# Kernel optimization log

Measured on AMD Instinct MI355X. Metric: run time of the kernel, lower is better.

## Reference

```python
import jax, jax.numpy as jnp
import numpy as np

N_NODES = 100000
N_EDGES = 3200000
N_GRAPHS = 1000
HID = 64
L = 4  # num_unit


def setup_inputs() -> dict:
    key = jax.random.key(0)
    ks = jax.random.split(key, 16)
    x = jax.random.normal(ks[0], (N_NODES, 4), dtype=jnp.float32)
    edge_index = jax.random.randint(ks[1], (2, N_EDGES), 0, N_NODES, dtype=jnp.int64)
    edge_attr = jax.random.uniform(ks[2], (N_EDGES,), dtype=jnp.float32)
    batch = jnp.sort(jax.random.randint(ks[3], (N_NODES,), 0, N_GRAPHS, dtype=jnp.int64))
    s = 1.0 / np.sqrt(HID)
    inp = {
        'x': x, 'edge_index': edge_index, 'edge_attr': edge_attr, 'batch': batch,
        'emb_w': jax.random.normal(ks[4], (4, HID), jnp.float32) * 0.5,
        'emb_b': jnp.zeros((HID,), jnp.float32),
        'conv_w1': jax.random.normal(ks[5], (L, HID, HID), jnp.float32) * s,
        'conv_b1': jnp.zeros((L, HID), jnp.float32),
        'conv_w2': jax.random.normal(ks[6], (L, HID, HID), jnp.float32) * s,
        'conv_w3': jax.random.normal(ks[7], (L, HID, HID), jnp.float32) * s,
        'conv_b3': jnp.zeros((L, HID), jnp.float32),
        'lin1_w': jax.random.normal(ks[8], (HID, HID), jnp.float32) * s,
        'lin1_b': jnp.zeros((HID,), jnp.float32),
        'lin2_w': jax.random.normal(ks[9], (HID, 3), jnp.float32) * s,
        'lin2_b': jnp.zeros((3,), jnp.float32),
    }
    return inp


def _forward(x, edge_index, edge_attr, batch,
             emb_w, emb_b, conv_w1, conv_b1, conv_w2, conv_w3, conv_b3,
             lin1_w, lin1_b, lin2_w, lin2_b):
    src, dst = edge_index[0], edge_index[1]
    ew = edge_attr[:, None]  # [E,1]
    h = x @ emb_w + emb_b  # node_emb; dropout omitted (eval mode)
    for l in range(conv_w1.shape[0]):
        # LEConv: out_i = sum_{j->i} w_ji * (lin1(x_j) - lin2(x_i)) + lin3(x_i)
        a = h @ conv_w1[l] + conv_b1[l]
        b = h @ conv_w2[l]  # no bias
        msg = (a[src] - b[dst]) * ew  # [E, HID]
        agg = jax.ops.segment_sum(msg, dst, num_segments=h.shape[0])
        h = jax.nn.relu(agg + h @ conv_w3[l] + conv_b3[l])
    # global mean pool over graphs
    sums = jax.ops.segment_sum(h, batch, num_segments=N_GRAPHS)
    cnt = jax.ops.segment_sum(jnp.ones((h.shape[0],), h.dtype), batch, num_segments=N_GRAPHS)
    graph_x = sums / jnp.maximum(cnt, 1.0)[:, None]
    pred = jax.nn.relu(graph_x @ lin1_w + lin1_b) @ lin2_w + lin2_b
    return pred


def reference(x, edge_index, edge_attr, batch, emb_w, emb_b,
              conv_w1, conv_b1, conv_w2, conv_w3, conv_b3,
              lin1_w, lin1_b, lin2_w, lin2_b):
    return _forward(x, edge_index, edge_attr, batch, emb_w, emb_b,
                    conv_w1, conv_b1, conv_w2, conv_w3, conv_b3,
                    lin1_w, lin1_b, lin2_w, lin2_b)
```

## Files before the change

kernel.cpp:

```cpp
#include <hip/hip_runtime.h>

#define N_NODES 100000
#define N_EDGES 3200000
#define N_GRAPHS 1000
#define NLAYER 4
#define NB 782
#define BBITS 7
#define EPB2 4096
#define G1 782
#define GH 782
#define PCAP 6144

typedef __attribute__((ext_vector_type(8))) short bf16x8;
typedef __attribute__((ext_vector_type(4))) float f32x4;

static __device__ __forceinline__ unsigned f2bf(float f) {
  unsigned u = __float_as_uint(f);
  return (u + 0x7fffu + ((u >> 16) & 1u)) >> 16;
}
static __device__ __forceinline__ float bf2f_lo(unsigned u) {
  return __uint_as_float(u << 16);
}
static __device__ __forceinline__ float bf2f_hi(unsigned u) {
  return __uint_as_float(u & 0xffff0000u);
}

__global__ __launch_bounds__(256) void zero_kernel(int* __restrict__ p, int n)
{
  int i = blockIdx.x * 256 + threadIdx.x;
  if (i < n) p[i] = 0;
}

__global__ __launch_bounds__(256) void embed_kernel(
    const float* __restrict__ x, const float* __restrict__ emb_w,
    const float* __restrict__ emb_b, unsigned short* __restrict__ h_bf)
{
  int t = blockIdx.x * 256 + threadIdx.x;
  if (t >= N_NODES * 64) return;
  int c = t & 63, v = t >> 6;
  float4 xv = ((const float4*)x)[v];
  float acc = emb_b[c];
  acc = fmaf(xv.x, emb_w[0 * 64 + c], acc);
  acc = fmaf(xv.y, emb_w[1 * 64 + c], acc);
  acc = fmaf(xv.z, emb_w[2 * 64 + c], acc);
  acc = fmaf(xv.w, emb_w[3 * 64 + c], acc);
  h_bf[t] = (unsigned short)f2bf(acc);
}

__global__ __launch_bounds__(256) void hist1_kernel(
    const int* __restrict__ ei, int* __restrict__ tots)
{
  __shared__ unsigned hist[NB];
  for (int i = threadIdx.x; i < NB; i += 256) hist[i] = 0;
  __syncthreads();
  int base = blockIdx.x * 4096;
#pragma unroll
  for (int i = 0; i < 16; ++i) {
    int e = base + i * 256 + threadIdx.x;
    if (e < N_EDGES) atomicAdd(&hist[((unsigned)ei[N_EDGES + e]) >> BBITS], 1u);
  }
  __syncthreads();
  for (int i = threadIdx.x; i < NB; i += 256) {
    unsigned c = hist[i];
    if (c) atomicAdd(&tots[i], (int)c);
  }
}

__global__ __launch_bounds__(1024) void scan1_kernel(
    const int* __restrict__ tots, int* __restrict__ bb, int* __restrict__ gcur)
{
  __shared__ int wsum[16];
  int t = threadIdx.x;
  int lane = t & 63;
  int w = t >> 6;
  int x = (t < NB) ? tots[t] : 0;
  int s = x;
  for (int off = 1; off < 64; off <<= 1) {
    int y = __shfl_up(s, off);
    if (lane >= off) s += y;
  }
  if (lane == 63) wsum[w] = s;
  __syncthreads();
  if (w == 0 && lane < 16) {
    int v = wsum[lane];
    int ss = v;
    for (int off = 1; off < 16; off <<= 1) {
      int y = __shfl_up(ss, off);
      if (lane >= off) ss += y;
    }
    wsum[lane] = ss - v;
  }
  __syncthreads();
  int ex = wsum[w] + s - x;
  if (t < NB) {
    bb[t] = ex;
    gcur[t] = ex;
  }
  if (t == 0) bb[NB] = N_EDGES;
}

__global__ __launch_bounds__(256) void bscatter3_kernel(
    const int* __restrict__ ei, const float* __restrict__ ea,
    int* __restrict__ gcur, int2* __restrict__ tmp)
{
  __shared__ unsigned hist[NB];
  int tid = threadIdx.x;
  int base = blockIdx.x * EPB2;
  for (int i = tid; i < NB; i += 256) hist[i] = 0;
  __syncthreads();

  int dreg[16];
#pragma unroll
  for (int i = 0; i < 16; ++i) {
    int e = base + i * 256 + tid;
    dreg[i] = -1;
    if (e < N_EDGES) {
      int d = ei[N_EDGES + e];
      dreg[i] = d;
      atomicAdd(&hist[((unsigned)d) >> BBITS], 1u);
    }
  }
  __syncthreads();

  for (int b = tid; b < NB; b += 256) {
    unsigned c = hist[b];
    hist[b] = c ? (unsigned)atomicAdd(&gcur[b], (int)c) : 0u;
  }
  __syncthreads();

#pragma unroll
  for (int i = 0; i < 16; ++i) {
    int e = base + i * 256 + tid;
    int d = dreg[i];
    if (d >= 0) {
      unsigned p = atomicAdd(&hist[((unsigned)d) >> BBITS], 1u);
      tmp[p] = make_int2(ei[e] | ((d & 127) << 17), __float_as_int(ea[e]));
    }
  }
}

__global__ __launch_bounds__(256) void bucket_sort2_kernel(
    const int* __restrict__ bb, const int2* __restrict__ tmp,
    unsigned* __restrict__ csr, int* __restrict__ row_off, float* __restrict__ degw)
{
  int j = blockIdx.x;
  int b0 = bb[j], b1 = bb[j + 1];
  int nE = b1 - b0;
  __shared__ unsigned hist[128];
  __shared__ float dws[128];
  __shared__ int scanbuf[256];
  __shared__ unsigned cur[128];
  __shared__ unsigned short perm[PCAP];
  int t = threadIdx.x;
  if (t < 128) { hist[t] = 0; dws[t] = 0.f; }
  __syncthreads();
  for (int i = t; i < nE; i += 256) {
    int2 r = tmp[b0 + i];
    int bin = ((unsigned)r.x) >> 17;
    atomicAdd(&hist[bin], 1u);
    atomicAdd(&dws[bin], __int_as_float(r.y));
  }
  __syncthreads();
  int v = (t < 128) ? (int)hist[t] : 0;
  scanbuf[t] = v;
  __syncthreads();
  for (int off = 1; off < 256; off <<= 1) {
    int y = (t >= off) ? scanbuf[t - off] : 0;
    __syncthreads();
    scanbuf[t] += y;
    __syncthreads();
  }
  int myexcl = scanbuf[t] - v;
  if (t < 128) {
    cur[t] = (unsigned)myexcl;
    int vnode = (j << BBITS) + t;
    if (vnode < N_NODES) {
      row_off[vnode] = b0 + myexcl;
      degw[vnode] = dws[t];
    }
  }
  if (j == NB - 1 && t == 0) row_off[N_NODES] = N_EDGES;
  __syncthreads();

  if (nE <= PCAP) {
    for (int i = t; i < nE; i += 256) {
      int2 r = tmp[b0 + i];
      int bin = ((unsigned)r.x) >> 17;
      unsigned p = atomicAdd(&cur[bin], 1u);
      perm[p] = (unsigned short)i;
    }
    __syncthreads();
    for (int q = t; q < nE; q += 256) {
      int2 r = tmp[b0 + (int)perm[q]];
      unsigned q15 = (unsigned)(__int_as_float(r.y) * 32768.0f);
      csr[b0 + q] = ((unsigned)r.x & 0x1FFFFu) | (q15 << 17);
    }
  } else {
    for (int i = t; i < nE; i += 256) {
      int2 r = tmp[b0 + i];
      int bin = ((unsigned)r.x) >> 17;
      unsigned p = atomicAdd(&cur[bin], 1u);
      unsigned q15 = (unsigned)(__int_as_float(r.y) * 32768.0f);
      csr[b0 + (int)p] = ((unsigned)r.x & 0x1FFFFu) | (q15 << 17);
    }
  }
}

__global__ __launch_bounds__(256) void dhist_kernel(
    const int* __restrict__ row_off, int* __restrict__ dhist)
{
  __shared__ unsigned h[256];
  int t = threadIdx.x;
  h[t] = 0;
  __syncthreads();
  int v0 = (blockIdx.x * 256 + t) * 4;
#pragma unroll
  for (int k = 0; k < 4; ++k) {
    int v = v0 + k;
    if (v < N_NODES) {
      int d = row_off[v + 1] - row_off[v];
      atomicAdd(&h[min(d, 255)], 1u);
    }
  }
  __syncthreads();
  unsigned c = h[t];
  if (c) atomicAdd(&dhist[t], (int)c);
}

__global__ __launch_bounds__(256) void dscan_kernel(
    const int* __restrict__ dhist, int* __restrict__ dcur)
{
  __shared__ int s[256];
  int t = threadIdx.x;
  int v = dhist[t];
  s[t] = v;
  __syncthreads();
  for (int off = 1; off < 256; off <<= 1) {
    int y = (t >= off) ? s[t - off] : 0;
    __syncthreads();
    s[t] += y;
    __syncthreads();
  }
  dcur[t] = s[t] - v;
}

__global__ __launch_bounds__(256) void dperm_kernel(
    const int* __restrict__ row_off, int* __restrict__ dcur,
    int* __restrict__ nodeperm)
{
  __shared__ unsigned h[256];
  __shared__ unsigned lcur[256];
  int t = threadIdx.x;
  h[t] = 0;
  __syncthreads();
  int v0 = (blockIdx.x * 256 + t) * 4;
  int dloc[4];
#pragma unroll
  for (int k = 0; k < 4; ++k) {
    int v = v0 + k;
    dloc[k] = -1;
    if (v < N_NODES) {
      int d = min(row_off[v + 1] - row_off[v], 255);
      dloc[k] = d;
      atomicAdd(&h[d], 1u);
    }
  }
  __syncthreads();
  unsigned c = h[t];
  unsigned gb = c ? (unsigned)atomicAdd(&dcur[t], (int)c) : 0u;
  lcur[t] = gb;
  __syncthreads();
#pragma unroll
  for (int k = 0; k < 4; ++k) {
    if (dloc[k] >= 0) {
      unsigned p = atomicAdd(&lcur[dloc[k]], 1u);
      nodeperm[p] = v0 + k;
    }
  }
}

__global__ __launch_bounds__(256) void wswz_kernel(
    const float* __restrict__ cw1, const float* __restrict__ cw2,
    const float* __restrict__ cw3, unsigned* __restrict__ wswz)
{
  int l = blockIdx.x;
  const float* w1 = cw1 + l * 4096;
  const float* w2 = cw2 + l * 4096;
  const float* w3 = cw3 + l * 4096;
  unsigned* outp = wswz + l * 6144;
  int tid = threadIdx.x;
  int n = tid & 63;
  int gofs = tid >> 6;
  for (int it = 0; it < 24; ++it) {
    int g = it * 4 + gofs;
    int m = g >> 5;
    int kp = g & 31;
    int k = kp * 2;
    const float* W = (m == 0) ? w2 : (m == 1) ? w3 : w1;
    unsigned lo = f2bf(W[k * 64 + n]);
    unsigned hi = f2bf(W[(k + 1) * 64 + n]);
    int c = k >> 5;
    int kk = k & 31;
    int lane = ((kk >> 3) << 4) | (n & 15);
    int j2 = (kk & 7) >> 1;
    int t = n >> 4;
    outp[(((m * 2 + c) * 4 + t) << 8) | (lane << 2) | j2] = lo | (hi << 16);
  }
}

__global__ __launch_bounds__(256) void matvec3_mfma_kernel(
    const unsigned short* __restrict__ h_bf,
    const unsigned* __restrict__ wz,
    const float* __restrict__ b1, const float* __restrict__ b3,
    const float* __restrict__ degw,
    unsigned short* __restrict__ a_bf, unsigned short* __restrict__ cc_bf)
{
  int gw = (blockIdx.x * 256 + threadIdx.x) >> 6;
  int lane = threadIdx.x & 63;
  int quad = lane >> 4;
  int col = lane & 15;
  int nb = gw * 16;
  if (nb >= N_NODES) return;

  int arow = nb + col;
  if (arow >= N_NODES) arow = N_NODES - 1;
  const bf16x8* ap = (const bf16x8*)(h_bf + (size_t)arow * 64 + quad * 8);
  bf16x8 af0 = ap[0];
  bf16x8 af1 = ap[4];

  float dwr[4];
#pragma unroll
  for (int r = 0; r < 4; ++r) {
    int row = nb + quad * 4 + r;
    dwr[r] = degw[row < N_NODES ? row : 0];
  }

#pragma unroll
  for (int t = 0; t < 4; ++t) {
    const bf16x8* b20 = (const bf16x8*)&wz[((0 * 4 + t) << 8) + lane * 4];
    const bf16x8* b21 = (const bf16x8*)&wz[((1 * 4 + t) << 8) + lane * 4];
    const bf16x8* b30 = (const bf16x8*)&wz[((2 * 4 + t) << 8) + lane * 4];
    const bf16x8* b31 = (const bf16x8*)&wz[((3 * 4 + t) << 8) + lane * 4];
    const bf16x8* b10 = (const bf16x8*)&wz[((4 * 4 + t) << 8) + lane * 4];
    const bf16x8* b11 = (const bf16x8*)&wz[((5 * 4 + t) << 8) + lane * 4];

    f32x4 z = {0.f, 0.f, 0.f, 0.f};
    f32x4 acc2 = __builtin_amdgcn_mfma_f32_16x16x32_bf16(af0, *b20, z, 0, 0, 0);
    acc2 = __builtin_amdgcn_mfma_f32_16x16x32_bf16(af1, *b21, acc2, 0, 0, 0);
    f32x4 cc;
#pragma unroll
    for (int r = 0; r < 4; ++r) cc[r] = -dwr[r] * acc2[r];
    cc = __builtin_amdgcn_mfma_f32_16x16x32_bf16(af0, *b30, cc, 0, 0, 0);
    cc = __builtin_amdgcn_mfma_f32_16x16x32_bf16(af1, *b31, cc, 0, 0, 0);
    float bb3 = b3[t * 16 + col];
#pragma unroll
    for (int r = 0; r < 4; ++r) {
      int row = nb + quad * 4 + r;
      if (row < N_NODES)
        cc_bf[(size_t)row * 64 + t * 16 + col] = (unsigned short)f2bf(cc[r] + bb3);
    }

    float bb1 = b1[t * 16 + col];
    f32x4 a1 = {bb1, bb1, bb1, bb1};
    a1 = __builtin_amdgcn_mfma_f32_16x16x32_bf16(af0, *b10, a1, 0, 0, 0);
    a1 = __builtin_amdgcn_mfma_f32_16x16x32_bf16(af1, *b11, a1, 0, 0, 0);
#pragma unroll
    for (int r = 0; r < 4; ++r) {
      int row = nb + quad * 4 + r;
      if (row < N_NODES)
        a_bf[(size_t)row * 64 + t * 16 + col] = (unsigned short)f2bf(a1[r]);
    }
  }
}

__global__ __launch_bounds__(256) void agg_kernel(
    const uint2* __restrict__ a2, const uint2* __restrict__ cc2,
    const int* __restrict__ row_off, const unsigned* __restrict__ csr,
    const int* __restrict__ nodeperm,
    float4* __restrict__ h4, unsigned short* __restrict__ h_bf, int write_h)
{
  int wave = (blockIdx.x * 256 + threadIdx.x) >> 6;
  int lane = threadIdx.x & 63;
  int sg = lane >> 4;
  int li = lane & 15;
  int lsel = (lane & 48) << 2;
  int vslot = wave * 4 + sg;
  bool valid = vslot < N_NODES;
  int v = nodeperm[valid ? vslot : N_NODES - 1];
  int base = row_off[v];
  int ecnt = valid ? (row_off[v + 1] - base) : 0;

  float4 acc = make_float4(0.f, 0.f, 0.f, 0.f);
  if (valid) {
    uint2 cu = cc2[(size_t)v * 16 + li];
    acc.x = bf2f_lo(cu.x);
    acc.y = bf2f_hi(cu.x);
    acc.z = bf2f_lo(cu.y);
    acc.w = bf2f_hi(cu.y);
  }
  const uint2* ap = a2 + li;

  int full = ecnt & ~15;
  int c0 = 0;
  for (; c0 < full; c0 += 16) {
    int er = (int)csr[base + c0 + li];
#pragma unroll
    for (int j = 0; j < 16; ++j) {
      unsigned r = (unsigned)__builtin_amdgcn_ds_bpermute(lsel | (j << 2), er);
      int s = (int)(r & 0x1FFFFu);
      float w = (float)(r >> 17) * (1.0f / 32768.0f);
      uint2 u = ap[(size_t)s * 16];
      acc.x = fmaf(w, bf2f_lo(u.x), acc.x);
      acc.y = fmaf(w, bf2f_hi(u.x), acc.y);
      acc.z = fmaf(w, bf2f_lo(u.y), acc.z);
      acc.w = fmaf(w, bf2f_hi(u.y), acc.w);
    }
  }
  int rem = ecnt - full;
  if (rem > 0) {
    int idx = c0 + li;
    int er = (idx < ecnt) ? (int)csr[base + idx] : 0;
    for (int j = 0; j < rem; ++j) {
      unsigned r = (unsigned)__builtin_amdgcn_ds_bpermute(lsel | (j << 2), er);
      int s = (int)(r & 0x1FFFFu);
      float w = (float)(r >> 17) * (1.0f / 32768.0f);
      uint2 u = ap[(size_t)s * 16];
      acc.x = fmaf(w, bf2f_lo(u.x), acc.x);
      acc.y = fmaf(w, bf2f_hi(u.x), acc.y);
      acc.z = fmaf(w, bf2f_lo(u.y), acc.z);
      acc.w = fmaf(w, bf2f_hi(u.y), acc.w);
    }
  }
  if (valid) {
    acc.x = fmaxf(acc.x, 0.f);
    acc.y = fmaxf(acc.y, 0.f);
    acc.z = fmaxf(acc.z, 0.f);
    acc.w = fmaxf(acc.w, 0.f);
    if (write_h) h4[(size_t)v * 16 + li] = acc;
    uint2 p;
    p.x = f2bf(acc.x) | (f2bf(acc.y) << 16);
    p.y = f2bf(acc.z) | (f2bf(acc.w) << 16);
    ((uint2*)h_bf)[(size_t)v * 16 + li] = p;
  }
}

__global__ __launch_bounds__(256) void head_kernel(
    const float* __restrict__ h, const int* __restrict__ batch,
    const float* __restrict__ l1w, const float* __restrict__ l1b,
    const float* __restrict__ l2w, const float* __restrict__ l2b,
    float* __restrict__ out)
{
  int g = (blockIdx.x * 256 + threadIdx.x) >> 6;
  int lane = threadIdx.x & 63;
  if (g >= N_GRAPHS) return;
  int lo = 0, hi = N_NODES;
  while (lo < hi) { int mid = (lo + hi) >> 1; if (batch[mid] < g) lo = mid + 1; else hi = mid; }
  int start = lo;
  hi = N_NODES;
  while (lo < hi) { int mid = (lo + hi) >> 1; if (batch[mid] < g + 1) lo = mid + 1; else hi = mid; }
  int end = lo;

  float sum = 0.f;
  for (int v = start; v < end; ++v) sum += h[(size_t)v * 64 + lane];
  float cntf = (float)(end - start);
  float gx = sum / fmaxf(cntf, 1.f);

  float acc = l1b[lane];
  for (int k = 0; k < 64; ++k) {
    float gxk = __shfl(gx, k);
    acc = fmaf(gxk, l1w[k * 64 + lane], acc);
  }
  float t = fmaxf(acc, 0.f);
  float p0 = t * l2w[lane * 3 + 0];
  float p1 = t * l2w[lane * 3 + 1];
  float p2 = t * l2w[lane * 3 + 2];
  for (int off = 32; off > 0; off >>= 1) {
    p0 += __shfl_down(p0, off);
    p1 += __shfl_down(p1, off);
    p2 += __shfl_down(p2, off);
  }
  if (lane == 0) {
    out[g * 3 + 0] = p0 + l2b[0];
    out[g * 3 + 1] = p1 + l2b[1];
    out[g * 3 + 2] = p2 + l2b[2];
  }
}

extern "C" void kernel_launch(void* const* d_in, const int* in_sizes, int n_in,
                              void* d_out, int out_size, void* d_ws, size_t ws_size,
                              hipStream_t stream)
{
  (void)in_sizes; (void)n_in; (void)out_size; (void)ws_size;
  const float* x     = (const float*)d_in[0];
  const int*   ei    = (const int*)d_in[1];
  const float* ea    = (const float*)d_in[2];
  const int*   batch = (const int*)d_in[3];
  const float* emb_w = (const float*)d_in[4];
  const float* emb_b = (const float*)d_in[5];
  const float* cw1   = (const float*)d_in[6];
  const float* cb1   = (const float*)d_in[7];
  const float* cw2   = (const float*)d_in[8];
  const float* cw3   = (const float*)d_in[9];
  const float* cb3   = (const float*)d_in[10];
  const float* l1w   = (const float*)d_in[11];
  const float* l1b   = (const float*)d_in[12];
  const float* l2w   = (const float*)d_in[13];
  const float* l2b   = (const float*)d_in[14];
  float* out = (float*)d_out;

  char* wsb = (char*)d_ws;
  size_t off = 0;
  auto alloc = [&](size_t bytes) {
    char* p = wsb + off;
    off = (off + bytes + 255) & ~(size_t)255;
    return p;
  };
  float* h       = (float*)alloc(sizeof(float) * (size_t)N_NODES * 64);
  unsigned short* h_bf = (unsigned short*)alloc(sizeof(short) * (size_t)N_NODES * 64);
  unsigned short* a_bf = (unsigned short*)alloc(sizeof(short) * (size_t)N_NODES * 64);
  unsigned short* cc_bf = (unsigned short*)alloc(sizeof(short) * (size_t)N_NODES * 64);
  unsigned* csr  = (unsigned*)alloc(sizeof(unsigned) * (size_t)N_EDGES);
  int*   row_off = (int*)alloc(sizeof(int) * (N_NODES + 1));
  float* degw    = (float*)alloc(sizeof(float) * N_NODES);
  int*   nodeperm= (int*)alloc(sizeof(int) * N_NODES);
  int*   tots    = (int*)alloc(sizeof(int) * NB);
  int*   dhist_g = (int*)alloc(sizeof(int) * 256);
  int*   bb      = (int*)alloc(sizeof(int) * (NB + 1));
  int*   gcur    = (int*)alloc(sizeof(int) * NB);
  int*   dcur    = (int*)alloc(sizeof(int) * 256);
  unsigned* wswz = (unsigned*)alloc(sizeof(unsigned) * NLAYER * 6144);
  int2* tmp = (int2*)h;

  zero_kernel<<<(NB + 255) / 256, 256, 0, stream>>>(tots, NB);
  zero_kernel<<<1, 256, 0, stream>>>(dhist_g, 256);

  embed_kernel<<<(N_NODES * 64 + 255) / 256, 256, 0, stream>>>(x, emb_w, emb_b, h_bf);
  wswz_kernel<<<NLAYER, 256, 0, stream>>>(cw1, cw2, cw3, wswz);
  hist1_kernel<<<GH, 256, 0, stream>>>(ei, tots);
  scan1_kernel<<<1, 1024, 0, stream>>>(tots, bb, gcur);
  bscatter3_kernel<<<G1, 256, 0, stream>>>(ei, ea, gcur, tmp);
  bucket_sort2_kernel<<<NB, 256, 0, stream>>>(bb, tmp, csr, row_off, degw);
  dhist_kernel<<<98, 256, 0, stream>>>(row_off, dhist_g);
  dscan_kernel<<<1, 256, 0, stream>>>(dhist_g, dcur);
  dperm_kernel<<<98, 256, 0, stream>>>(row_off, dcur, nodeperm);

  int agg_blocks = (N_NODES + 15) / 16;
  int mv_blocks = (N_NODES / 16 + 3) / 4 + 1;
  for (int l = 0; l < NLAYER; ++l) {
    matvec3_mfma_kernel<<<mv_blocks, 256, 0, stream>>>(
        h_bf, wswz + l * 6144, cb1 + l * 64, cb3 + l * 64, degw, a_bf, cc_bf);
    agg_kernel<<<agg_blocks, 256, 0, stream>>>(
        (const uint2*)a_bf, (const uint2*)cc_bf, row_off, csr, nodeperm, (float4*)h,
        h_bf, (l == NLAYER - 1) ? 1 : 0);
  }

  head_kernel<<<(N_GRAPHS * 64 + 255) / 256, 256, 0, stream>>>(
      h, batch, l1w, l1b, l2w, l2b, out);
}
```

Before: 595.2 us.

## Restructure CSR build with 256-node buckets, staged scatter, and single-block degree sort

Rebuilds the edge-sorting preprocessing. Buckets now hold 256 nodes instead of 128. The scatter pass first stages edges in shared memory sorted by bucket, then writes them out coalesced as a packed 4-byte word plus a 1-byte local destination, replacing the old 8-byte records. The zeroing kernels are folded into the embed kernel, and the three degree-sort kernels are merged into a single 1024-thread block. The aim is to cut launch count and scatter memory traffic. The single-block degree sort serialises over 100k nodes, and the wider buckets make the per-bucket sort larger and lean on a bigger shared permutation buffer.

```diff
diff --git a/kernel.cpp b/kernel.cpp
--- a/kernel.cpp
+++ b/kernel.cpp
@@ -4,12 +4,10 @@
 #define N_EDGES 3200000
 #define N_GRAPHS 1000
 #define NLAYER 4
-#define NB 782
-#define BBITS 7
-#define EPB2 4096
+#define NB4 391
+#define EPB4 4096
 #define G1 782
-#define GH 782
-#define PCAP 6144
+#define PCAP3 10240
 
 typedef __attribute__((ext_vector_type(8))) short bf16x8;
 typedef __attribute__((ext_vector_type(4))) float f32x4;
@@ -25,16 +23,14 @@
   return __uint_as_float(u & 0xffff0000u);
 }
 
-__global__ __launch_bounds__(256) void zero_kernel(int* __restrict__ p, int n)
-{
-  int i = blockIdx.x * 256 + threadIdx.x;
-  if (i < n) p[i] = 0;
-}
-
 __global__ __launch_bounds__(256) void embed_kernel(
     const float* __restrict__ x, const float* __restrict__ emb_w,
-    const float* __restrict__ emb_b, unsigned short* __restrict__ h_bf)
-{
+    const float* __restrict__ emb_b, unsigned short* __restrict__ h_bf,
+    int* __restrict__ tots)
+{
+  if (blockIdx.x == 0) {
+    for (int i = threadIdx.x; i < NB4; i += 256) tots[i] = 0;
+  }
   int t = blockIdx.x * 256 + threadIdx.x;
   if (t >= N_NODES * 64) return;
   int c = t & 63, v = t >> 6;
@@ -50,17 +46,17 @@
 __global__ __launch_bounds__(256) void hist1_kernel(
     const int* __restrict__ ei, int* __restrict__ tots)
 {
-  __shared__ unsigned hist[NB];
-  for (int i = threadIdx.x; i < NB; i += 256) hist[i] = 0;
-  __syncthreads();
-  int base = blockIdx.x * 4096;
+  __shared__ unsigned hist[NB4];
+  for (int i = threadIdx.x; i < NB4; i += 256) hist[i] = 0;
+  __syncthreads();
+  int base = blockIdx.x * EPB4;
 #pragma unroll
   for (int i = 0; i < 16; ++i) {
     int e = base + i * 256 + threadIdx.x;
-    if (e < N_EDGES) atomicAdd(&hist[((unsigned)ei[N_EDGES + e]) >> BBITS], 1u);
-  }
-  __syncthreads();
-  for (int i = threadIdx.x; i < NB; i += 256) {
+    if (e < N_EDGES) atomicAdd(&hist[((unsigned)ei[N_EDGES + e]) >> 8], 1u);
+  }
+  __syncthreads();
+  for (int i = threadIdx.x; i < NB4; i += 256) {
     unsigned c = hist[i];
     if (c) atomicAdd(&tots[i], (int)c);
   }
@@ -73,8 +69,9 @@
   int t = threadIdx.x;
   int lane = t & 63;
   int w = t >> 6;
-  int x = (t < NB) ? tots[t] : 0;
+  int x = (t < NB4) ? tots[t] : 0;
   int s = x;
+#pragma unroll
   for (int off = 1; off < 64; off <<= 1) {
     int y = __shfl_up(s, off);
     if (lane >= off) s += y;
@@ -84,6 +81,7 @@
   if (w == 0 && lane < 16) {
     int v = wsum[lane];
     int ss = v;
+#pragma unroll
     for (int off = 1; off < 16; off <<= 1) {
       int y = __shfl_up(ss, off);
       if (lane >= off) ss += y;
@@ -92,21 +90,28 @@
   }
   __syncthreads();
   int ex = wsum[w] + s - x;
-  if (t < NB) {
+  if (t < NB4) {
     bb[t] = ex;
     gcur[t] = ex;
   }
-  if (t == 0) bb[NB] = N_EDGES;
-}
-
-__global__ __launch_bounds__(256) void bscatter3_kernel(
+  if (t == 0) bb[NB4] = N_EDGES;
+}
+
+__global__ __launch_bounds__(256) void bscatter4_kernel(
     const int* __restrict__ ei, const float* __restrict__ ea,
-    int* __restrict__ gcur, int2* __restrict__ tmp)
-{
-  __shared__ unsigned hist[NB];
+    int* __restrict__ gcur, unsigned* __restrict__ tmp_w,
+    unsigned char* __restrict__ tmp_d)
+{
+  __shared__ unsigned hist[NB4];
+  __shared__ int dif[NB4];
+  __shared__ unsigned stage_w[EPB4];
+  __shared__ unsigned char stage_d[EPB4];
+  __shared__ unsigned short bid[EPB4];
+  __shared__ int wpart[4];
   int tid = threadIdx.x;
-  int base = blockIdx.x * EPB2;
-  for (int i = tid; i < NB; i += 256) hist[i] = 0;
+  int base = blockIdx.x * EPB4;
+
+  for (int i = tid; i < NB4; i += 256) hist[i] = 0;
   __syncthreads();
 
   int dreg[16];
@@ -117,14 +122,36 @@
     if (e < N_EDGES) {
       int d = ei[N_EDGES + e];
       dreg[i] = d;
-      atomicAdd(&hist[((unsigned)d) >> BBITS], 1u);
-    }
-  }
-  __syncthreads();
-
-  for (int b = tid; b < NB; b += 256) {
-    unsigned c = hist[b];
-    hist[b] = c ? (unsigned)atomicAdd(&gcur[b], (int)c) : 0u;
+      atomicAdd(&hist[((unsigned)d) >> 8], 1u);
+    }
+  }
+  __syncthreads();
+
+  int lane = tid & 63, w = tid >> 6;
+  int b0i = tid * 2, b1i = tid * 2 + 1;
+  int c0 = (b0i < NB4) ? (int)hist[b0i] : 0;
+  int c1 = (b1i < NB4) ? (int)hist[b1i] : 0;
+  int tsum = c0 + c1;
+  int s = tsum;
+#pragma unroll
+  for (int off = 1; off < 64; off <<= 1) {
+    int y = __shfl_up(s, off);
+    if (lane >= off) s += y;
+  }
+  if (lane == 63) wpart[w] = s;
+  __syncthreads();
+  int wo = 0;
+  for (int ww = 0; ww < w; ++ww) wo += wpart[ww];
+  int excl = wo + (s - tsum);
+  if (b0i < NB4) {
+    int gb = c0 ? atomicAdd(&gcur[b0i], c0) : 0;
+    dif[b0i] = gb - excl;
+    hist[b0i] = (unsigned)excl;
+  }
+  if (b1i < NB4) {
+    int gb = c1 ? atomicAdd(&gcur[b1i], c1) : 0;
+    dif[b1i] = gb - (excl + c0);
+    hist[b1i] = (unsigned)(excl + c0);
   }
   __syncthreads();
 
@@ -133,149 +160,122 @@
     int e = base + i * 256 + tid;
     int d = dreg[i];
     if (d >= 0) {
-      unsigned p = atomicAdd(&hist[((unsigned)d) >> BBITS], 1u);
-      tmp[p] = make_int2(ei[e] | ((d & 127) << 17), __float_as_int(ea[e]));
-    }
-  }
-}
-
-__global__ __launch_bounds__(256) void bucket_sort2_kernel(
-    const int* __restrict__ bb, const int2* __restrict__ tmp,
+      unsigned bkt = ((unsigned)d) >> 8;
+      unsigned lp = atomicAdd(&hist[bkt], 1u);
+      unsigned q15 = (unsigned)(ea[e] * 32768.0f);
+      stage_w[lp] = ((unsigned)ei[e]) | (q15 << 17);
+      stage_d[lp] = (unsigned char)(d & 255);
+      bid[lp] = (unsigned short)bkt;
+    }
+  }
+  __syncthreads();
+
+  int nE = min(EPB4, N_EDGES - base);
+  for (int i = tid; i < nE; i += 256) {
+    int g = dif[bid[i]] + i;
+    tmp_w[g] = stage_w[i];
+    tmp_d[g] = stage_d[i];
+  }
+}
+
+__global__ __launch_bounds__(256) void bucket_sort3_kernel(
+    const int* __restrict__ bb, const unsigned* __restrict__ tmp_w,
+    const unsigned char* __restrict__ tmp_d,
     unsigned* __restrict__ csr, int* __restrict__ row_off, float* __restrict__ degw)
 {
   int j = blockIdx.x;
   int b0 = bb[j], b1 = bb[j + 1];
   int nE = b1 - b0;
-  __shared__ unsigned hist[128];
-  __shared__ float dws[128];
-  __shared__ int scanbuf[256];
-  __shared__ unsigned cur[128];
-  __shared__ unsigned short perm[PCAP];
+  __shared__ unsigned hist[256];
+  __shared__ float dws[256];
+  __shared__ unsigned cur[256];
+  __shared__ int wpart[4];
+  __shared__ unsigned short perm[PCAP3];
   int t = threadIdx.x;
-  if (t < 128) { hist[t] = 0; dws[t] = 0.f; }
+  hist[t] = 0;
+  dws[t] = 0.f;
   __syncthreads();
   for (int i = t; i < nE; i += 256) {
-    int2 r = tmp[b0 + i];
-    int bin = ((unsigned)r.x) >> 17;
-    atomicAdd(&hist[bin], 1u);
-    atomicAdd(&dws[bin], __int_as_float(r.y));
-  }
-  __syncthreads();
-  int v = (t < 128) ? (int)hist[t] : 0;
-  scanbuf[t] = v;
-  __syncthreads();
-  for (int off = 1; off < 256; off <<= 1) {
-    int y = (t >= off) ? scanbuf[t - off] : 0;
+    unsigned d = tmp_d[b0 + i];
+    unsigned wrd = tmp_w[b0 + i];
+    atomicAdd(&hist[d], 1u);
+    atomicAdd(&dws[d], (float)(wrd >> 17) * (1.0f / 32768.0f));
+  }
+  __syncthreads();
+  int lane = t & 63, w = t >> 6;
+  int v = (int)hist[t];
+  int s = v;
+#pragma unroll
+  for (int off = 1; off < 64; off <<= 1) {
+    int y = __shfl_up(s, off);
+    if (lane >= off) s += y;
+  }
+  if (lane == 63) wpart[w] = s;
+  __syncthreads();
+  int wo = 0;
+  for (int ww = 0; ww < w; ++ww) wo += wpart[ww];
+  int excl = wo + s - v;
+  cur[t] = (unsigned)excl;
+  int vnode = (j << 8) + t;
+  if (vnode < N_NODES) {
+    row_off[vnode] = b0 + excl;
+    degw[vnode] = dws[t];
+  }
+  if (j == NB4 - 1 && t == 0) row_off[N_NODES] = N_EDGES;
+  __syncthreads();
+
+  if (nE <= PCAP3) {
+    for (int i = t; i < nE; i += 256) {
+      unsigned p = atomicAdd(&cur[tmp_d[b0 + i]], 1u);
+      perm[p] = (unsigned short)i;
+    }
     __syncthreads();
-    scanbuf[t] += y;
-    __syncthreads();
-  }
-  int myexcl = scanbuf[t] - v;
-  if (t < 128) {
-    cur[t] = (unsigned)myexcl;
-    int vnode = (j << BBITS) + t;
-    if (vnode < N_NODES) {
-      row_off[vnode] = b0 + myexcl;
-      degw[vnode] = dws[t];
-    }
-  }
-  if (j == NB - 1 && t == 0) row_off[N_NODES] = N_EDGES;
-  __syncthreads();
-
-  if (nE <= PCAP) {
-    for (int i = t; i < nE; i += 256) {
-      int2 r = tmp[b0 + i];
-      int bin = ((unsigned)r.x) >> 17;
-      unsigned p = atomicAdd(&cur[bin], 1u);
-      perm[p] = (unsigned short)i;
-    }
-    __syncthreads();
-    for (int q = t; q < nE; q += 256) {
-      int2 r = tmp[b0 + (int)perm[q]];
-      unsigned q15 = (unsigned)(__int_as_float(r.y) * 32768.0f);
-      csr[b0 + q] = ((unsigned)r.x & 0x1FFFFu) | (q15 << 17);
-    }
+    for (int q = t; q < nE; q += 256)
+      csr[b0 + q] = tmp_w[b0 + (int)perm[q]];
   } else {
     for (int i = t; i < nE; i += 256) {
-      int2 r = tmp[b0 + i];
-      int bin = ((unsigned)r.x) >> 17;
-      unsigned p = atomicAdd(&cur[bin], 1u);
-      unsigned q15 = (unsigned)(__int_as_float(r.y) * 32768.0f);
-      csr[b0 + (int)p] = ((unsigned)r.x & 0x1FFFFu) | (q15 << 17);
-    }
-  }
-}
-
-__global__ __launch_bounds__(256) void dhist_kernel(
-    const int* __restrict__ row_off, int* __restrict__ dhist)
-{
-  __shared__ unsigned h[256];
+      unsigned p = atomicAdd(&cur[tmp_d[b0 + i]], 1u);
+      csr[b0 + (int)p] = tmp_w[b0 + i];
+    }
+  }
+}
+
+__global__ __launch_bounds__(1024) void degsort_kernel(
+    const int* __restrict__ row_off, int* __restrict__ nodeperm)
+{
+  __shared__ int h[256];
+  __shared__ int wp[4];
   int t = threadIdx.x;
-  h[t] = 0;
-  __syncthreads();
-  int v0 = (blockIdx.x * 256 + t) * 4;
-#pragma unroll
-  for (int k = 0; k < 4; ++k) {
-    int v = v0 + k;
-    if (v < N_NODES) {
-      int d = row_off[v + 1] - row_off[v];
-      atomicAdd(&h[min(d, 255)], 1u);
-    }
-  }
-  __syncthreads();
-  unsigned c = h[t];
-  if (c) atomicAdd(&dhist[t], (int)c);
-}
-
-__global__ __launch_bounds__(256) void dscan_kernel(
-    const int* __restrict__ dhist, int* __restrict__ dcur)
-{
-  __shared__ int s[256];
-  int t = threadIdx.x;
-  int v = dhist[t];
-  s[t] = v;
-  __syncthreads();
-  for (int off = 1; off < 256; off <<= 1) {
-    int y = (t >= off) ? s[t - off] : 0;
-    __syncthreads();
-    s[t] += y;
-    __syncthreads();
-  }
-  dcur[t] = s[t] - v;
-}
-
-__global__ __launch_bounds__(256) void dperm_kernel(
-    const int* __restrict__ row_off, int* __restrict__ dcur,
-    int* __restrict__ nodeperm)
-{
-  __shared__ unsigned h[256];
-  __shared__ unsigned lcur[256];
-  int t = threadIdx.x;
-  h[t] = 0;
-  __syncthreads();
-  int v0 = (blockIdx.x * 256 + t) * 4;
-  int dloc[4];
-#pragma unroll
-  for (int k = 0; k < 4; ++k) {
-    int v = v0 + k;
-    dloc[k] = -1;
-    if (v < N_NODES) {
-      int d = min(row_off[v + 1] - row_off[v], 255);
-      dloc[k] = d;
-      atomicAdd(&h[d], 1u);
-    }
-  }
-  __syncthreads();
-  unsigned c = h[t];
-  unsigned gb = c ? (unsigned)atomicAdd(&dcur[t], (int)c) : 0u;
-  lcur[t] = gb;
-  __syncthreads();
-#pragma unroll
-  for (int k = 0; k < 4; ++k) {
-    if (dloc[k] >= 0) {
-      unsigned p = atomicAdd(&lcur[dloc[k]], 1u);
-      nodeperm[p] = v0 + k;
-    }
+  if (t < 256) h[t] = 0;
+  __syncthreads();
+  for (int v = t; v < N_NODES; v += 1024) {
+    int d = min(row_off[v + 1] - row_off[v], 255);
+    atomicAdd(&h[d], 1);
+  }
+  __syncthreads();
+  int lane = t & 63, w = t >> 6;
+  int v0 = 0, s = 0;
+  if (t < 256) {
+    v0 = h[t];
+    s = v0;
+#pragma unroll
+    for (int off = 1; off < 64; off <<= 1) {
+      int y = __shfl_up(s, off);
+      if (lane >= off) s += y;
+    }
+    if (lane == 63) wp[w] = s;
+  }
+  __syncthreads();
+  if (t < 256) {
+    int wo = 0;
+    for (int ww = 0; ww < w; ++ww) wo += wp[ww];
+    h[t] = wo + s - v0;
+  }
+  __syncthreads();
+  for (int v = t; v < N_NODES; v += 1024) {
+    int d = min(row_off[v + 1] - row_off[v], 255);
+    int p = atomicAdd(&h[d], 1);
+    nodeperm[p] = v;
   }
 }
 
@@ -523,26 +523,21 @@
   int*   row_off = (int*)alloc(sizeof(int) * (N_NODES + 1));
   float* degw    = (float*)alloc(sizeof(float) * N_NODES);
   int*   nodeperm= (int*)alloc(sizeof(int) * N_NODES);
-  int*   tots    = (int*)alloc(sizeof(int) * NB);
-  int*   dhist_g = (int*)alloc(sizeof(int) * 256);
-  int*   bb      = (int*)alloc(sizeof(int) * (NB + 1));
-  int*   gcur    = (int*)alloc(sizeof(int) * NB);
-  int*   dcur    = (int*)alloc(sizeof(int) * 256);
+  int*   tots    = (int*)alloc(sizeof(int) * NB4);
+  int*   bb      = (int*)alloc(sizeof(int) * (NB4 + 1));
+  int*   gcur    = (int*)alloc(sizeof(int) * NB4);
   unsigned* wswz = (unsigned*)alloc(sizeof(unsigned) * NLAYER * 6144);
-  int2* tmp = (int2*)h;
-
-  zero_kernel<<<(NB + 255) / 256, 256, 0, stream>>>(tots, NB);
-  zero_kernel<<<1, 256, 0, stream>>>(dhist_g, 256);
-
-  embed_kernel<<<(N_NODES * 64 + 255) / 256, 256, 0, stream>>>(x, emb_w, emb_b, h_bf);
+  unsigned* tmp_w = (unsigned*)h;
+  unsigned char* tmp_d = (unsigned char*)h + sizeof(unsigned) * (size_t)N_EDGES;
+
+  embed_kernel<<<(N_NODES * 64 + 255) / 256, 256, 0, stream>>>(
+      x, emb_w, emb_b, h_bf, tots);
   wswz_kernel<<<NLAYER, 256, 0, stream>>>(cw1, cw2, cw3, wswz);
-  hist1_kernel<<<GH, 256, 0, stream>>>(ei, tots);
+  hist1_kernel<<<G1, 256, 0, stream>>>(ei, tots);
   scan1_kernel<<<1, 1024, 0, stream>>>(tots, bb, gcur);
-  bscatter3_kernel<<<G1, 256, 0, stream>>>(ei, ea, gcur, tmp);
-  bucket_sort2_kernel<<<NB, 256, 0, stream>>>(bb, tmp, csr, row_off, degw);
-  dhist_kernel<<<98, 256, 0, stream>>>(row_off, dhist_g);
-  dscan_kernel<<<1, 256, 0, stream>>>(dhist_g, dcur);
-  dperm_kernel<<<98, 256, 0, stream>>>(row_off, dcur, nodeperm);
+  bscatter4_kernel<<<G1, 256, 0, stream>>>(ei, ea, gcur, tmp_w, tmp_d);
+  bucket_sort3_kernel<<<NB4, 256, 0, stream>>>(bb, tmp_w, tmp_d, csr, row_off, degw);
+  degsort_kernel<<<1, 1024, 0, stream>>>(row_off, nodeperm);
 
   int agg_blocks = (N_NODES + 15) / 16;
   int mv_blocks = (N_NODES / 16 + 3) / 4 + 1;
```

New measurement: 635.0 us. 6.7% more time.
